# Kernel tuning notes

Measured on AMD Instinct MI355X. Metric: run time of the kernel, lower is better.

## Reference

```python
import jax, jax.numpy as jnp
import numpy as np
import math

D_MODEL = 256
N_HEADS = 8
N_LEVELS = 4
N_POINTS = 4
D_HEAD = D_MODEL // N_HEADS
SPATIAL_SHAPES = np.array([[64, 64], [32, 32], [16, 16], [8, 8]], dtype=np.int64)


def _offset_bias():
    # faithful to MSDeformAttn._reset_parameters grid init for sampling_offsets bias
    thetas = np.arange(N_HEADS, dtype=np.float32) * (2.0 * math.pi / N_HEADS)
    grid = np.stack([np.cos(thetas), np.sin(thetas)], -1)
    grid = grid / np.abs(grid).max(-1, keepdims=True)
    grid = np.tile(grid[:, None, None, :], (1, N_LEVELS, N_POINTS, 1)).copy()
    for i in range(N_POINTS):
        grid[:, :, i, :] *= i + 1
    return jnp.asarray(grid.reshape(-1), jnp.float32)


def setup_inputs() -> dict:
    key = jax.random.key(0)
    ks = jax.random.split(key, 8)
    N, Q = 2, 10000
    areas = SPATIAL_SHAPES[:, 0] * SPATIAL_SHAPES[:, 1]
    len_in = int(areas.sum())
    lsi = np.concatenate([[0], np.cumsum(areas)[:-1]])
    s = 1.0 / float(np.sqrt(D_MODEL))
    return {
        "query": jax.random.normal(ks[0], (N, Q, D_MODEL), jnp.float32),
        "reference_points": jax.random.uniform(ks[1], (N, Q, N_LEVELS, 2), jnp.float32),
        "input_flatten": jax.random.normal(ks[2], (N, len_in, D_MODEL), jnp.float32),
        "input_spatial_shapes": jnp.asarray(SPATIAL_SHAPES, jnp.int32),
        "input_level_start_index": jnp.asarray(lsi, jnp.int32),
        "W_value": jax.random.normal(ks[3], (D_MODEL, D_MODEL), jnp.float32) * s,
        "b_value": jnp.zeros((D_MODEL,), jnp.float32),
        "W_off": jax.random.normal(ks[4], (D_MODEL, N_HEADS * N_LEVELS * N_POINTS * 2), jnp.float32) * 0.01,
        "b_off": _offset_bias(),
        "W_attn": jax.random.normal(ks[5], (D_MODEL, N_HEADS * N_LEVELS * N_POINTS), jnp.float32) * 0.01,
        "b_attn": jnp.zeros((N_HEADS * N_LEVELS * N_POINTS,), jnp.float32),
        "W_out": jax.random.normal(ks[6], (D_MODEL, D_MODEL), jnp.float32) * s,
        "b_out": jnp.zeros((D_MODEL,), jnp.float32),
    }


def _bilinear(val, loc, H, W):
    # val: (B, H*W, d); loc: (B, S, 2) in [0,1]; matches F.grid_sample(align_corners=False, padding_mode='zeros')
    x = loc[..., 0] * W - 0.5
    y = loc[..., 1] * H - 0.5
    x0f = jnp.floor(x)
    y0f = jnp.floor(y)
    wx = (x - x0f)[..., None]
    wy = (y - y0f)[..., None]
    x0 = x0f.astype(jnp.int32)
    y0 = y0f.astype(jnp.int32)

    def gather(xi, yi):
        valid = ((xi >= 0) & (xi < W) & (yi >= 0) & (yi < H))[..., None]
        idx = jnp.clip(yi, 0, H - 1) * W + jnp.clip(xi, 0, W - 1)
        return jnp.take_along_axis(val, idx[..., None], axis=1) * valid

    v00 = gather(x0, y0)
    v01 = gather(x0 + 1, y0)
    v10 = gather(x0, y0 + 1)
    v11 = gather(x0 + 1, y0 + 1)
    return v00 * (1 - wx) * (1 - wy) + v01 * wx * (1 - wy) + v10 * (1 - wx) * wy + v11 * wx * wy


def _forward(query, reference_points, input_flatten, W_value, b_value, W_off, b_off, W_attn, b_attn, W_out, b_out):
    N, Q, _ = query.shape
    value = (input_flatten @ W_value + b_value).reshape(N, -1, N_HEADS, D_HEAD)
    off = (query @ W_off + b_off).reshape(N, Q, N_HEADS, N_LEVELS, N_POINTS, 2)
    attn = jax.nn.softmax((query @ W_attn + b_attn).reshape(N, Q, N_HEADS, N_LEVELS * N_POINTS), axis=-1)
    attn = attn.reshape(N, Q, N_HEADS, N_LEVELS, N_POINTS)
    # offset normalizer is (W_l, H_l) per level
    norm = jnp.asarray(np.stack([SPATIAL_SHAPES[:, 1], SPATIAL_SHAPES[:, 0]], -1), query.dtype)
    loc = reference_points[:, :, None, :, None, :] + off / norm[None, None, None, :, None, :]
    start = 0
    sampled = []
    for l in range(N_LEVELS):
        H_, W_ = int(SPATIAL_SHAPES[l, 0]), int(SPATIAL_SHAPES[l, 1])
        val_l = value[:, start:start + H_ * W_]  # (N, HW, nH, d)
        val_l = val_l.transpose(0, 2, 1, 3).reshape(N * N_HEADS, H_ * W_, D_HEAD)
        loc_l = loc[:, :, :, l].transpose(0, 2, 1, 3, 4).reshape(N * N_HEADS, Q * N_POINTS, 2)
        s_l = _bilinear(val_l, loc_l, H_, W_).reshape(N, N_HEADS, Q, N_POINTS, D_HEAD)
        sampled.append(s_l)
        start += H_ * W_
    sampled = jnp.stack(sampled, axis=3)  # (N, nH, Q, L, P, d)
    out = jnp.einsum('nhqlpd,nqhlp->nqhd', sampled, attn).reshape(N, Q, D_MODEL)
    return out @ W_out + b_out


def reference(query, reference_points, input_flatten, input_spatial_shapes, input_level_start_index, W_value, b_value, W_off, b_off, W_attn, b_attn, W_out, b_out):
    # input_spatial_shapes / input_level_start_index are static metadata (SPATIAL_SHAPES)
    return _forward(query, reference_points, input_flatten, W_value, b_value, W_off, b_off, W_attn, b_attn, W_out, b_out)
```

## Files before the change

### kernel.cpp

```cpp
#include <hip/hip_runtime.h>

#define NB 2
#define NQ 10000
#define DM 256
#define NHEADS 8
#define NLEV 4
#define NPTS 4
#define DHEAD 32
#define LEN_IN 5440

typedef _Float16 f16x8 __attribute__((ext_vector_type(8)));
typedef _Float16 f16x4 __attribute__((ext_vector_type(4)));
typedef float    f32x4 __attribute__((ext_vector_type(4)));
typedef unsigned short u16x4 __attribute__((ext_vector_type(4)));

union TaskU {
    struct { f16x4 w; u16x4 p; } s;
    uint4 u;
};

__device__ __forceinline__ void swz_one(const float* __restrict__ W, int Nw,
                                        int srcCol, int kbase,
                                        _Float16* __restrict__ dst) {
    f16x8 v;
    #pragma unroll
    for (int j = 0; j < 8; ++j) v[j] = (_Float16)W[(size_t)(kbase + j) * Nw + srcCol];
    *(f16x8*)dst = v;
}

__global__ __launch_bounds__(256) void prep(const float* __restrict__ Wv,
                                            const float* __restrict__ Wo,
                                            const float* __restrict__ Wa,
                                            const float* __restrict__ Wout,
                                            const float* __restrict__ query,
                                            const float* __restrict__ inflat,
                                            _Float16* __restrict__ Wv_swz,
                                            _Float16* __restrict__ Wofa_swz,
                                            _Float16* __restrict__ Wout_swz,
                                            _Float16* __restrict__ query_h,
                                            _Float16* __restrict__ inflat_h) {
    const int b = blockIdx.x;
    const int t = threadIdx.x;
    if (b < 112) {
        const int tid = b * 256 + t;
        if (tid < 8192) {
            const int lane = tid & 63, tt = tid >> 6, kt = tt & 7, nt = tt >> 3;
            swz_one(Wv, 256, nt * 16 + (lane & 15), kt * 32 + (lane >> 4) * 8,
                    Wv_swz + ((size_t)(nt * 8 + kt) * 64 + lane) * 8);
        } else if (tid < 16384) {
            const int local = tid - 8192;
            const int lane = local & 63, tt = local >> 6, kt = tt & 7, nt = tt >> 3;
            swz_one(Wo, 256, nt * 16 + (lane & 15), kt * 32 + (lane >> 4) * 8,
                    Wofa_swz + ((size_t)(nt * 8 + kt) * 64 + lane) * 8);
        } else if (tid < 20480) {
            const int local = tid - 16384;
            const int lane = local & 63, tt = local >> 6, kt = tt & 7, nt = tt >> 3;
            swz_one(Wa, 128, nt * 16 + (lane & 15), kt * 32 + (lane >> 4) * 8,
                    Wofa_swz + ((size_t)((16 + nt) * 8 + kt) * 64 + lane) * 8);
        } else if (tid < 28672) {
            const int local = tid - 20480;
            const int lane = local & 63, tt = local >> 6, kt = tt & 7, nt = tt >> 3;
            swz_one(Wout, 256, nt * 16 + (lane & 15), kt * 32 + (lane >> 4) * 8,
                    Wout_swz + ((size_t)(nt * 8 + kt) * 64 + lane) * 8);
        }
    } else if (b < 112 + 2500) {
        const size_t e = ((size_t)(b - 112) * 256 + t) * 8;
        const float4 lo = *(const float4*)(query + e);
        const float4 hi = *(const float4*)(query + e + 4);
        f16x8 o;
        o[0] = (_Float16)lo.x; o[1] = (_Float16)lo.y; o[2] = (_Float16)lo.z; o[3] = (_Float16)lo.w;
        o[4] = (_Float16)hi.x; o[5] = (_Float16)hi.y; o[6] = (_Float16)hi.z; o[7] = (_Float16)hi.w;
        *(f16x8*)(query_h + e) = o;
    } else {
        const size_t e = ((size_t)(b - 2612) * 256 + t) * 8;
        const float4 lo = *(const float4*)(inflat + e);
        const float4 hi = *(const float4*)(inflat + e + 4);
        f16x8 o;
        o[0] = (_Float16)lo.x; o[1] = (_Float16)lo.y; o[2] = (_Float16)lo.z; o[3] = (_Float16)lo.w;
        o[4] = (_Float16)hi.x; o[5] = (_Float16)hi.y; o[6] = (_Float16)hi.z; o[7] = (_Float16)hi.w;
        *(f16x8*)(inflat_h + e) = o;
    }
}

template<int OUTMODE>
__device__ __forceinline__ void tile_gemm(const _Float16* __restrict__ A,
                                          const _Float16* __restrict__ Wswz,
                                          const float* __restrict__ bias0,
                                          const float* __restrict__ bias1,
                                          int bsplit,
                                          void* __restrict__ C_,
                                          int M, int N, int mb, int nb) {
    const int lane = threadIdx.x & 63;
    const int w = threadIdx.x >> 6;
    const int wm = w & 1, wn = w >> 1;
    const int m0 = mb + wm * 32;
    const int n0 = nb + wn * 32;
    const int r = lane & 15;
    const int klane = (lane >> 4) * 8;
    const int rc0 = min(m0 + r, M - 1);
    const int rc1 = min(m0 + 16 + r, M - 1);
    const int ntile0 = n0 >> 4;

    f32x4 acc[2][2] = {};
    #pragma unroll
    for (int kt = 0; kt < 8; ++kt) {
        const f16x8 a0 = *(const f16x8*)(A + (size_t)rc0 * 256 + kt * 32 + klane);
        const f16x8 a1 = *(const f16x8*)(A + (size_t)rc1 * 256 + kt * 32 + klane);
        const f16x8 b0 = *(const f16x8*)(Wswz + ((size_t)((ntile0 + 0) * 8 + kt) * 64 + lane) * 8);
        const f16x8 b1 = *(const f16x8*)(Wswz + ((size_t)((ntile0 + 1) * 8 + kt) * 64 + lane) * 8);
        acc[0][0] = __builtin_amdgcn_mfma_f32_16x16x32_f16(a0, b0, acc[0][0], 0, 0, 0);
        acc[0][1] = __builtin_amdgcn_mfma_f32_16x16x32_f16(a0, b1, acc[0][1], 0, 0, 0);
        acc[1][0] = __builtin_amdgcn_mfma_f32_16x16x32_f16(a1, b0, acc[1][0], 0, 0, 0);
        acc[1][1] = __builtin_amdgcn_mfma_f32_16x16x32_f16(a1, b1, acc[1][1], 0, 0, 0);
    }
    #pragma unroll
    for (int j = 0; j < 2; ++j) {
        const int col = n0 + j * 16 + r;
        const float bb = (col < bsplit) ? bias0[col] : bias1[col - bsplit];
        #pragma unroll
        for (int i = 0; i < 2; ++i) {
            #pragma unroll
            for (int rr = 0; rr < 4; ++rr) {
                const int row = m0 + i * 16 + (lane >> 4) * 4 + rr;
                if (row < M) {
                    const float v = acc[i][j][rr] + bb;
                    if constexpr (OUTMODE == 0) {
                        ((_Float16*)C_)[(size_t)row * N + col] = (_Float16)v;
                    } else {
                        const int n_img = row >= LEN_IN;
                        const int pix = row - (n_img ? LEN_IN : 0);
                        ((_Float16*)C_)[((((size_t)(n_img * 8 + (col >> 5)) * LEN_IN) + pix) << 5)
                                        + (col & 31)] = (_Float16)v;
                    }
                }
            }
        }
    }
}

__global__ __launch_bounds__(256) void gemm_front(const _Float16* __restrict__ inflat_h,
                                                  const _Float16* __restrict__ query_h,
                                                  const _Float16* __restrict__ Wv_swz,
                                                  const _Float16* __restrict__ Wofa_swz,
                                                  const float* __restrict__ b_value,
                                                  const float* __restrict__ b_off,
                                                  const float* __restrict__ b_attn,
                                                  _Float16* __restrict__ value_h,
                                                  _Float16* __restrict__ ofa_h) {
    const int bx = blockIdx.x;
    if (bx < 680) {
        tile_gemm<2>(inflat_h, Wv_swz, b_value, b_value, 256, value_h,
                     NB * LEN_IN, 256, (bx % 170) * 64, (bx / 170) * 64);
    } else {
        const int b2 = bx - 680;
        tile_gemm<0>(query_h, Wofa_swz, b_off, b_attn, 256, ofa_h,
                     NB * NQ, 384, (b2 % 313) * 64, (b2 / 313) * 64);
    }
}

__device__ __forceinline__ f16x8 sp8(_Float16 w) {
    return (f16x8){w, w, w, w, w, w, w, w};
}

__global__ __launch_bounds__(512) void sample_out(const float* __restrict__ refp,
                                                  const _Float16* __restrict__ ofa,
                                                  const _Float16* __restrict__ value,
                                                  const _Float16* __restrict__ Wout_swz,
                                                  const float* __restrict__ b_out,
                                                  float* __restrict__ out) {
    __shared__ float attns_s[16][128];
    __shared__ float refs[16][NLEV][2];
    __shared__ uint4 tasks[2048];
    uint4* oplds = (uint4*)&attns_s[0][0];

    const int t = threadIdx.x;
    const int xcd = blockIdx.x & 7;
    const int slot = blockIdx.x >> 3;
    const int n = xcd >> 2;
    const int grp = slot * 4 + (xcd & 3);
    if (grp >= NQ / 16) return;
    const int q0 = grp * 16;
    const size_t qb = (size_t)n * NQ + q0;

    if (t < 128) {
        {
            const int i = t >> 3, rem = t & 7;
            refs[i][rem >> 1][rem & 1] = refp[(qb + i) * NLEV * 2 + rem];
        }
        const int q = t >> 3, h = t & 7;
        const _Float16* arow = ofa + (qb + q) * 384 + 256 + h * 16;
        const f16x8 a0 = *(const f16x8*)arow;
        const f16x8 a1 = *(const f16x8*)(arow + 8);
        float a[16];
        #pragma unroll
        for (int j = 0; j < 8; ++j) { a[j] = (float)a0[j]; a[8 + j] = (float)a1[j]; }
        float m = a[0];
        #pragma unroll
        for (int j = 1; j < 16; ++j) m = fmaxf(m, a[j]);
        float s = 0.f;
        #pragma unroll
        for (int j = 0; j < 16; ++j) { const float e = __expf(a[j] - m); a[j] = e; s += e; }
        const float inv = 1.0f / s;
        #pragma unroll
        for (int j = 0; j < 16; ++j) attns_s[q][h * 16 + j] = a[j] * inv;
    }
    __syncthreads();

    {
        const int q = t >> 5, h = (t >> 2) & 7, lvl = t & 3, qh = t >> 2;
        constexpr int HS[4] = {64, 32, 16, 8};
        constexpr int ST[4] = {0, 4096, 5120, 5376};
        const int H_ = HS[lvl], W_ = HS[lvl], st = ST[lvl];
        const float fW = (float)W_, fH = (float)H_;
        const float invW = 1.0f / fW, invH = 1.0f / fH;
        const float rx = refs[q][lvl][0];
        const float ry = refs[q][lvl][1];
        const f16x8 off8 = *(const f16x8*)(ofa + (qb + q) * 384 + (h * 16 + lvl * 4) * 2);
        const f32x4 at4 = *(const f32x4*)&attns_s[q][h * 16 + lvl * 4];
        #pragma unroll
        for (int pt = 0; pt < NPTS; ++pt) {
            const float lx = rx + (float)off8[pt * 2]     * invW;
            const float ly = ry + (float)off8[pt * 2 + 1] * invH;
            const float aw = at4[pt];
            const float x = lx * fW - 0.5f;
            const float y = ly * fH - 0.5f;
            const float x0f = floorf(x);
            const float y0f = floorf(y);
            const float wx = x - x0f;
            const float wy = y - y0f;
            const int x0 = (int)x0f, y0 = (int)y0f;
            const int x1 = x0 + 1, y1 = y0 + 1;
            const int xc0 = min(max(x0, 0), W_ - 1);
            const int xc1 = min(max(x1, 0), W_ - 1);
            const int yc0 = min(max(y0, 0), H_ - 1);
            const int yc1 = min(max(y1, 0), H_ - 1);
            const bool vx0 = (x0 >= 0) & (x0 < W_);
            const bool vx1 = (x1 >= 0) & (x1 < W_);
            const bool vy0 = (y0 >= 0) & (y0 < H_);
            const bool vy1 = (y1 >= 0) & (y1 < H_);
            const float w00 = (vx0 & vy0) ? aw * (1.f - wx) * (1.f - wy) : 0.f;
            const float w01 = (vx1 & vy0) ? aw * wx         * (1.f - wy) : 0.f;
            const float w10 = (vx0 & vy1) ? aw * (1.f - wx) * wy         : 0.f;
            const float w11 = (vx1 & vy1) ? aw * wx         * wy         : 0.f;
            TaskU tu;
            tu.s.w = (f16x4){(_Float16)w00, (_Float16)w01, (_Float16)w10, (_Float16)w11};
            tu.s.p = (u16x4){(unsigned short)(st + yc0 * W_ + xc0),
                             (unsigned short)(st + yc0 * W_ + xc1),
                             (unsigned short)(st + yc1 * W_ + xc0),
                             (unsigned short)(st + yc1 * W_ + xc1)};
            tasks[qh * 16 + ((lvl * 4 + pt) ^ (qh & 15))] = tu.u;
        }
    }
    __syncthreads();

    {
        const int q = t >> 5, h = (t >> 2) & 7, g = t & 3, qh = t >> 2;
        const _Float16* vhead = value + ((size_t)(n * 8 + h) * LEN_IN) * 32 + g * 8;
        f16x8 acc = {};
        #pragma unroll 4
        for (int ptIdx = 0; ptIdx < 16; ++ptIdx) {
            TaskU tu;
            tu.u = tasks[qh * 16 + (ptIdx ^ (qh & 15))];
            const f16x8 v0 = *(const f16x8*)(vhead + ((size_t)tu.s.p[0] << 5));
            const f16x8 v1 = *(const f16x8*)(vhead + ((size_t)tu.s.p[1] << 5));
            const f16x8 v2 = *(const f16x8*)(vhead + ((size_t)tu.s.p[2] << 5));
            const f16x8 v3 = *(const f16x8*)(vhead + ((size_t)tu.s.p[3] << 5));
            acc += v0 * sp8(tu.s.w[0]);
            acc += v1 * sp8(tu.s.w[1]);
            acc += v2 * sp8(tu.s.w[2]);
            acc += v3 * sp8(tu.s.w[3]);
        }
        const int byte = q * 512 + ((h * 64 + g * 16) ^ ((q & 7) << 4));
        *(f16x8*)((char*)oplds + byte) = acc;
    }
    __syncthreads();

    {
        const int lane = t & 63;
        const int w = t >> 6;
        const int r = lane & 15;
        const int kq = lane >> 4;
        f32x4 acc[2] = {};
        #pragma unroll
        for (int kt = 0; kt < 8; ++kt) {
            const int abyte = r * 512 + ((kt * 64 + kq * 16) ^ ((r & 7) << 4));
            const f16x8 a = *(const f16x8*)((const char*)oplds + abyte);
            #pragma unroll
            for (int nt = 0; nt < 2; ++nt) {
                const int ntile = w * 2 + nt;
                const f16x8 b = *(const f16x8*)(Wout_swz + ((size_t)(ntile * 8 + kt) * 64 + lane) * 8);
                acc[nt] = __builtin_amdgcn_mfma_f32_16x16x32_f16(a, b, acc[nt], 0, 0, 0);
            }
        }
        #pragma unroll
        for (int nt = 0; nt < 2; ++nt) {
            const int col = (w * 2 + nt) * 16 + r;
            const float bb = b_out[col];
            #pragma unroll
            for (int rr = 0; rr < 4; ++rr) {
                const int row = kq * 4 + rr;
                out[(qb + row) * 256 + col] = acc[nt][rr] + bb;
            }
        }
    }
}

extern "C" void kernel_launch(void* const* d_in, const int* in_sizes, int n_in,
                              void* d_out, int out_size, void* d_ws, size_t ws_size,
                              hipStream_t stream) {
    const float* query  = (const float*)d_in[0];
    const float* refp   = (const float*)d_in[1];
    const float* inflat = (const float*)d_in[2];
    const float* W_value = (const float*)d_in[5];
    const float* b_value = (const float*)d_in[6];
    const float* W_off   = (const float*)d_in[7];
    const float* b_off   = (const float*)d_in[8];
    const float* W_attn  = (const float*)d_in[9];
    const float* b_attn  = (const float*)d_in[10];
    const float* W_out   = (const float*)d_in[11];
    const float* b_out   = (const float*)d_in[12];
    float* out = (float*)d_out;

    char* ws = (char*)d_ws;
    _Float16* value_h   = (_Float16*)(ws);
    _Float16* ofa_h     = (_Float16*)(ws + 5570560);
    _Float16* Wv_swz    = (_Float16*)(ws + 20930560);
    _Float16* Wofa_swz  = (_Float16*)(ws + 21061632);
    _Float16* Wout_swz  = (_Float16*)(ws + 31170560);
    _Float16* query_h   = (_Float16*)((char*)d_out);
    _Float16* inflat_h  = (_Float16*)((char*)d_out + 10240000);

    prep<<<3972, 256, 0, stream>>>(W_value, W_off, W_attn, W_out, query, inflat,
                                   Wv_swz, Wofa_swz, Wout_swz, query_h, inflat_h);
    gemm_front<<<2558, 256, 0, stream>>>(inflat_h, query_h, Wv_swz, Wofa_swz,
                                         b_value, b_off, b_attn, value_h, ofa_h);
    sample_out<<<1280, 512, 0, stream>>>(refp, ofa_h, value_h, Wout_swz,
                                         b_out, out);
}
```

Measured before the change: 77.23 us.

## Fuse offset/attention projection GEMM into sampling kernel via shared memory

Moves the query projection (sampling offsets and attention logits) from the front GEMM kernel into the sampling kernel. Each block now computes its 16 queries' 384-column projection with MFMA straight from fp32 query into shared memory. This removes the query fp16 conversion pass and the global write and reread of the ofa intermediate. In exchange, the sampling kernel does more work per block and uses more shared memory. Attention weights are now kept in fp16 in shared memory, and a launch-bounds occupancy hint is added.

```diff
diff --git a/kernel.cpp b/kernel.cpp
--- a/kernel.cpp
+++ b/kernel.cpp
@@ -32,12 +32,10 @@
                                             const float* __restrict__ Wo,
                                             const float* __restrict__ Wa,
                                             const float* __restrict__ Wout,
-                                            const float* __restrict__ query,
                                             const float* __restrict__ inflat,
                                             _Float16* __restrict__ Wv_swz,
                                             _Float16* __restrict__ Wofa_swz,
                                             _Float16* __restrict__ Wout_swz,
-                                            _Float16* __restrict__ query_h,
                                             _Float16* __restrict__ inflat_h) {
     const int b = blockIdx.x;
     const int t = threadIdx.x;
@@ -63,16 +61,8 @@
             swz_one(Wout, 256, nt * 16 + (lane & 15), kt * 32 + (lane >> 4) * 8,
                     Wout_swz + ((size_t)(nt * 8 + kt) * 64 + lane) * 8);
         }
-    } else if (b < 112 + 2500) {
+    } else {
         const size_t e = ((size_t)(b - 112) * 256 + t) * 8;
-        const float4 lo = *(const float4*)(query + e);
-        const float4 hi = *(const float4*)(query + e + 4);
-        f16x8 o;
-        o[0] = (_Float16)lo.x; o[1] = (_Float16)lo.y; o[2] = (_Float16)lo.z; o[3] = (_Float16)lo.w;
-        o[4] = (_Float16)hi.x; o[5] = (_Float16)hi.y; o[6] = (_Float16)hi.z; o[7] = (_Float16)hi.w;
-        *(f16x8*)(query_h + e) = o;
-    } else {
-        const size_t e = ((size_t)(b - 2612) * 256 + t) * 8;
         const float4 lo = *(const float4*)(inflat + e);
         const float4 hi = *(const float4*)(inflat + e + 4);
         f16x8 o;
@@ -82,14 +72,13 @@
     }
 }
 
-template<int OUTMODE>
-__device__ __forceinline__ void tile_gemm(const _Float16* __restrict__ A,
-                                          const _Float16* __restrict__ Wswz,
-                                          const float* __restrict__ bias0,
-                                          const float* __restrict__ bias1,
-                                          int bsplit,
-                                          void* __restrict__ C_,
-                                          int M, int N, int mb, int nb) {
+__global__ __launch_bounds__(256) void gemm_value(const _Float16* __restrict__ A,
+                                                  const _Float16* __restrict__ Wswz,
+                                                  const float* __restrict__ bias,
+                                                  _Float16* __restrict__ C) {
+    const int mb = (blockIdx.x % 170) * 64;
+    const int nb = (blockIdx.x / 170) * 64;
+    const int M = NB * LEN_IN;
     const int lane = threadIdx.x & 63;
     const int w = threadIdx.x >> 6;
     const int wm = w & 1, wn = w >> 1;
@@ -116,45 +105,20 @@
     #pragma unroll
     for (int j = 0; j < 2; ++j) {
         const int col = n0 + j * 16 + r;
-        const float bb = (col < bsplit) ? bias0[col] : bias1[col - bsplit];
+        const float bb = bias[col];
         #pragma unroll
         for (int i = 0; i < 2; ++i) {
             #pragma unroll
             for (int rr = 0; rr < 4; ++rr) {
                 const int row = m0 + i * 16 + (lane >> 4) * 4 + rr;
                 if (row < M) {
-                    const float v = acc[i][j][rr] + bb;
-                    if constexpr (OUTMODE == 0) {
-                        ((_Float16*)C_)[(size_t)row * N + col] = (_Float16)v;
-                    } else {
-                        const int n_img = row >= LEN_IN;
-                        const int pix = row - (n_img ? LEN_IN : 0);
-                        ((_Float16*)C_)[((((size_t)(n_img * 8 + (col >> 5)) * LEN_IN) + pix) << 5)
-                                        + (col & 31)] = (_Float16)v;
-                    }
+                    const int n_img = row >= LEN_IN;
+                    const int pix = row - (n_img ? LEN_IN : 0);
+                    C[((((size_t)(n_img * 8 + (col >> 5)) * LEN_IN) + pix) << 5)
+                      + (col & 31)] = (_Float16)(acc[i][j][rr] + bb);
                 }
             }
         }
-    }
-}
-
-__global__ __launch_bounds__(256) void gemm_front(const _Float16* __restrict__ inflat_h,
-                                                  const _Float16* __restrict__ query_h,
-                                                  const _Float16* __restrict__ Wv_swz,
-                                                  const _Float16* __restrict__ Wofa_swz,
-                                                  const float* __restrict__ b_value,
-                                                  const float* __restrict__ b_off,
-                                                  const float* __restrict__ b_attn,
-                                                  _Float16* __restrict__ value_h,
-                                                  _Float16* __restrict__ ofa_h) {
-    const int bx = blockIdx.x;
-    if (bx < 680) {
-        tile_gemm<2>(inflat_h, Wv_swz, b_value, b_value, 256, value_h,
-                     NB * LEN_IN, 256, (bx % 170) * 64, (bx / 170) * 64);
-    } else {
-        const int b2 = bx - 680;
-        tile_gemm<0>(query_h, Wofa_swz, b_off, b_attn, 256, ofa_h,
-                     NB * NQ, 384, (b2 % 313) * 64, (b2 / 313) * 64);
     }
 }
 
@@ -162,16 +126,19 @@
     return (f16x8){w, w, w, w, w, w, w, w};
 }
 
-__global__ __launch_bounds__(512) void sample_out(const float* __restrict__ refp,
-                                                  const _Float16* __restrict__ ofa,
-                                                  const _Float16* __restrict__ value,
-                                                  const _Float16* __restrict__ Wout_swz,
-                                                  const float* __restrict__ b_out,
-                                                  float* __restrict__ out) {
-    __shared__ float attns_s[16][128];
+__global__ __launch_bounds__(512, 6) void sample_out(const float* __restrict__ query,
+                                                     const float* __restrict__ refp,
+                                                     const _Float16* __restrict__ Wofa_swz,
+                                                     const float* __restrict__ b_off,
+                                                     const float* __restrict__ b_attn,
+                                                     const _Float16* __restrict__ value,
+                                                     const _Float16* __restrict__ Wout_swz,
+                                                     const float* __restrict__ b_out,
+                                                     float* __restrict__ out) {
+    __shared__ _Float16 ofa_s[16][384];
     __shared__ float refs[16][NLEV][2];
     __shared__ uint4 tasks[2048];
-    uint4* oplds = (uint4*)&attns_s[0][0];
+    uint4* oplds = (uint4*)&ofa_s[0][0];
 
     const int t = threadIdx.x;
     const int xcd = blockIdx.x & 7;
@@ -182,18 +149,50 @@
     const int q0 = grp * 16;
     const size_t qb = (size_t)n * NQ + q0;
 
+    {
+        const int lane = t & 63;
+        const int w = t >> 6;
+        const int r = lane & 15;
+        const int klane = (lane >> 4) * 8;
+        const float* qrow = query + (qb + r) * 256 + klane;
+        f32x4 acc[3] = {};
+        #pragma unroll
+        for (int kt = 0; kt < 8; ++kt) {
+            const float4 lo = *(const float4*)(qrow + kt * 32);
+            const float4 hi = *(const float4*)(qrow + kt * 32 + 4);
+            f16x8 a;
+            a[0] = (_Float16)lo.x; a[1] = (_Float16)lo.y; a[2] = (_Float16)lo.z; a[3] = (_Float16)lo.w;
+            a[4] = (_Float16)hi.x; a[5] = (_Float16)hi.y; a[6] = (_Float16)hi.z; a[7] = (_Float16)hi.w;
+            #pragma unroll
+            for (int nt = 0; nt < 3; ++nt) {
+                const int ntile = w * 3 + nt;
+                const f16x8 b = *(const f16x8*)(Wofa_swz + ((size_t)(ntile * 8 + kt) * 64 + lane) * 8);
+                acc[nt] = __builtin_amdgcn_mfma_f32_16x16x32_f16(a, b, acc[nt], 0, 0, 0);
+            }
+        }
+        #pragma unroll
+        for (int nt = 0; nt < 3; ++nt) {
+            const int col = (w * 3 + nt) * 16 + r;
+            const float bb = (col < 256) ? b_off[col] : b_attn[col - 256];
+            #pragma unroll
+            for (int rr = 0; rr < 4; ++rr) {
+                const int q = (lane >> 4) * 4 + rr;
+                ofa_s[q][col] = (_Float16)(acc[nt][rr] + bb);
+            }
+        }
+    }
+    __syncthreads();
+
     if (t < 128) {
         {
             const int i = t >> 3, rem = t & 7;
             refs[i][rem >> 1][rem & 1] = refp[(qb + i) * NLEV * 2 + rem];
         }
         const int q = t >> 3, h = t & 7;
-        const _Float16* arow = ofa + (qb + q) * 384 + 256 + h * 16;
-        const f16x8 a0 = *(const f16x8*)arow;
-        const f16x8 a1 = *(const f16x8*)(arow + 8);
+        _Float16* arow = &ofa_s[q][256 + h * 16];
         float a[16];
         #pragma unroll
-        for (int j = 0; j < 8; ++j) { a[j] = (float)a0[j]; a[8 + j] = (float)a1[j]; }
+        for (int j = 0; j < 16; ++j) a[j] = (float)arow[j];
         float m = a[0];
         #pragma unroll
         for (int j = 1; j < 16; ++j) m = fmaxf(m, a[j]);
@@ -202,7 +201,7 @@
         for (int j = 0; j < 16; ++j) { const float e = __expf(a[j] - m); a[j] = e; s += e; }
         const float inv = 1.0f / s;
         #pragma unroll
-        for (int j = 0; j < 16; ++j) attns_s[q][h * 16 + j] = a[j] * inv;
+        for (int j = 0; j < 16; ++j) arow[j] = (_Float16)(a[j] * inv);
     }
     __syncthreads();
 
@@ -215,13 +214,13 @@
         const float invW = 1.0f / fW, invH = 1.0f / fH;
         const float rx = refs[q][lvl][0];
         const float ry = refs[q][lvl][1];
-        const f16x8 off8 = *(const f16x8*)(ofa + (qb + q) * 384 + (h * 16 + lvl * 4) * 2);
-        const f32x4 at4 = *(const f32x4*)&attns_s[q][h * 16 + lvl * 4];
+        const f16x8 off8 = *(const f16x8*)&ofa_s[q][(h * 16 + lvl * 4) * 2];
+        const f16x4 at4 = *(const f16x4*)&ofa_s[q][256 + h * 16 + lvl * 4];
         #pragma unroll
         for (int pt = 0; pt < NPTS; ++pt) {
             const float lx = rx + (float)off8[pt * 2]     * invW;
             const float ly = ry + (float)off8[pt * 2 + 1] * invH;
-            const float aw = at4[pt];
+            const float aw = (float)at4[pt];
             const float x = lx * fW - 0.5f;
             const float y = ly * fH - 0.5f;
             const float x0f = floorf(x);
@@ -323,17 +322,14 @@
 
     char* ws = (char*)d_ws;
     _Float16* value_h   = (_Float16*)(ws);
-    _Float16* ofa_h     = (_Float16*)(ws + 5570560);
     _Float16* Wv_swz    = (_Float16*)(ws + 20930560);
     _Float16* Wofa_swz  = (_Float16*)(ws + 21061632);
     _Float16* Wout_swz  = (_Float16*)(ws + 31170560);
-    _Float16* query_h   = (_Float16*)((char*)d_out);
-    _Float16* inflat_h  = (_Float16*)((char*)d_out + 10240000);
-
-    prep<<<3972, 256, 0, stream>>>(W_value, W_off, W_attn, W_out, query, inflat,
-                                   Wv_swz, Wofa_swz, Wout_swz, query_h, inflat_h);
-    gemm_front<<<2558, 256, 0, stream>>>(inflat_h, query_h, Wv_swz, Wofa_swz,
-                                         b_value, b_off, b_attn, value_h, ofa_h);
-    sample_out<<<1280, 512, 0, stream>>>(refp, ofa_h, value_h, Wout_swz,
-                                         b_out, out);
-}
+    _Float16* inflat_h  = (_Float16*)((char*)d_out);
+
+    prep<<<1472, 256, 0, stream>>>(W_value, W_off, W_attn, W_out, inflat,
+                                   Wv_swz, Wofa_swz, Wout_swz, inflat_h);
+    gemm_value<<<680, 256, 0, stream>>>(inflat_h, Wv_swz, b_value, value_h);
+    sample_out<<<1280, 512, 0, stream>>>(query, refp, Wofa_swz, b_off, b_attn,
+                                         value_h, Wout_swz, b_out, out);
+}
```

After: 79.07 us. +2.4%, slower.
